# Kernel tuning notes

Hardware: AMD Instinct MI355X
Metric: run time of the kernel (lower is better)

## Reference

```python
import jax, jax.numpy as jnp
import numpy as np
import math

N = 30000        # nodes
E = 390000       # edges (first N are self-loops, in node order)
H = 64
NNS = 4          # num_node_states
NES = 4          # num_edge_states
NGRAPH = 64      # graphs in batch
TEMP_ON_EVAL = 1.0


def from_binary(bits):
    # bits: [..., k] of {0,1} -> integer code sum(bits * 2^k)
    pw = (2 ** jnp.arange(bits.shape[-1])).astype(bits.dtype)
    return jnp.sum(bits * pw, axis=-1)


def segment_softmax(logits, seg, num_seg, tau):
    m = jax.ops.segment_max(logits, seg, num_segments=num_seg)
    e = jnp.exp((logits - m[seg]) / tau)
    s = jax.ops.segment_sum(e, seg, num_segments=num_seg)
    return e / s[seg]


def segment_hard_onehot(logits, seg, num_seg):
    # gumbel_softmax with tau=0, no noise: one-hot at per-segment argmax (first on ties)
    n = logits.shape[0]
    m = jax.ops.segment_max(logits, seg, num_segments=num_seg)
    idx = jnp.where(logits >= m[seg], jnp.arange(n, dtype=jnp.int32), jnp.int32(n))
    first = jax.ops.segment_min(idx, seg, num_segments=num_seg)
    return (jnp.arange(n, dtype=jnp.int32) == first[seg]).astype(jnp.int32)


def select_best(emb, bits, scalars, index, num_index):
    # SelectBest with use_select_best=True. states are even ints < 2^(k+1);
    # unique((states, index)) groups == fused key states*num_index+index.
    states = 2 * from_binary(bits)
    key = states * num_index + index
    num_key = (2 ** (bits.shape[-1] + 1)) * num_index
    best = segment_hard_onehot(-scalars[:, 0], key, num_key)
    return emb[states + best]


def temp_by_step(step, upper, lower, num_iter, temp_on_eval):
    if step == -1:
        return temp_on_eval
    frac = min(float(step) / num_iter, 1.0)
    return upper + (lower - upper) * frac


def forward(node_states, edge_states, scalars, edge_index, batch_vec, rev_idx,
            emb_edge, emb_sbv, emb_sbr, emb_static,
            Wq, Wk, Wv, Wek, Wev, Wc, training_step):
    ei0, ei1 = edge_index[0], edge_index[1]
    # self-loop edges are the first N edges in node order ->
    # scalars[edge_index[0]==edge_index[1]] == scalars[:N]
    node_scalars = scalars[:N]                                   # [N,1]

    # select_best_from_virtual
    node_fts = select_best(emb_sbv, node_states, node_scalars, batch_vec, NGRAPH)  # [N,H]
    edge_fts = emb_edge[from_binary(edge_states)]                # [E,H]

    Q = node_fts @ Wq.T
    K = node_fts @ Wk.T
    V = node_fts @ Wv.T

    # combined_edge_KV
    sb = select_best(emb_sbr, node_states[ei0], scalars, ei1, N)  # [E,H]
    edge_K = sb @ Wek.T
    sender_s = node_scalars[ei0]                                  # [E,1]
    reciever_s = node_scalars[ei1]                                # [E,1]
    rlx = (scalars < reciever_s)
    rlx_d = (sender_s + scalars < reciever_s)
    fts = jnp.concatenate([rlx, rlx_d], axis=-1).astype(jnp.int32)  # [E,2] bits
    static_fts = emb_static[from_binary(fts)]                     # [E,H]
    combined = jnp.concatenate([edge_fts, edge_fts[rev_idx], static_fts], axis=1)  # [E,3H]
    edge_V = combined @ Wc.T                                      # [E,H]

    # compute_message
    Qe = Q[ei1]
    Ke = K[ei0] + edge_K
    Ve = V[ei0] + edge_V
    alpha = jnp.sum(Qe * Ke, axis=-1) / math.sqrt(H)              # [E]
    tau = temp_by_step(int(training_step), 3.0, 0.1, 10000, TEMP_ON_EVAL)
    alpha = segment_softmax(alpha, ei1, N, tau)
    message = Ve * alpha[:, None]                                  # [E,H]

    node_out = node_fts + jax.ops.segment_sum(message, ei1, num_segments=N)
    edge_out = edge_fts + message
    return node_out, edge_out


def setup_inputs() -> dict:
    key = jax.random.key(0)
    ks = jax.random.split(key, 16)
    node_states = jax.random.randint(ks[0], (N, NNS), 0, 2, dtype=jnp.int32)
    edge_states = jax.random.randint(ks[1], (E, NES), 0, 2, dtype=jnp.int32)
    scalars = jax.random.normal(ks[2], (E, 1), dtype=jnp.float32)
    loops = jnp.arange(N, dtype=jnp.int32)
    senders = jax.random.randint(ks[3], (E - N,), 0, N, dtype=jnp.int32)
    receivers = jax.random.randint(ks[4], (E - N,), 0, N, dtype=jnp.int32)
    edge_index = jnp.stack([jnp.concatenate([loops, senders]),
                            jnp.concatenate([loops, receivers])])  # [2,E]
    batch_vec = jnp.sort(jax.random.randint(ks[5], (N,), 0, NGRAPH, dtype=jnp.int32))
    rev_idx = jax.random.permutation(ks[6], E).astype(jnp.int32)
    s = 0.05
    return {
        'node_states': node_states, 'edge_states': edge_states, 'scalars': scalars,
        'edge_index': edge_index, 'batch_vec': batch_vec, 'rev_idx': rev_idx,
        'emb_edge': s * jax.random.normal(ks[7], (2 ** NES, H), dtype=jnp.float32),
        'emb_sbv': s * jax.random.normal(ks[8], (2 ** (NNS + 1), H), dtype=jnp.float32),
        'emb_sbr': s * jax.random.normal(ks[9], (2 ** (NNS + 1), H), dtype=jnp.float32),
        'emb_static': s * jax.random.normal(ks[10], (4, H), dtype=jnp.float32),
        'Wq': s * jax.random.normal(ks[11], (H, H), dtype=jnp.float32),
        'Wk': s * jax.random.normal(ks[12], (H, H), dtype=jnp.float32),
        'Wv': s * jax.random.normal(ks[13], (H, H), dtype=jnp.float32),
        'Wek': s * jax.random.normal(ks[14], (H, H), dtype=jnp.float32),
        'Wev': s * jax.random.normal(ks[15], (H, H), dtype=jnp.float32),
        'Wc': s * jax.random.normal(jax.random.fold_in(key, 99), (H, 3 * H), dtype=jnp.float32),
        'training_step': -1,
    }


def reference(node_states, edge_states, scalars, edge_index, batch_vec, rev_idx,
              emb_edge, emb_sbv, emb_sbr, emb_static,
              Wq, Wk, Wv, Wek, Wev, Wc, training_step):
    return forward(node_states, edge_states, scalars, edge_index, batch_vec, rev_idx,
                   emb_edge, emb_sbv, emb_sbr, emb_static,
                   Wq, Wk, Wv, Wek, Wev, Wc, training_step)
```

## Files before the change

kernel.cpp:

```cpp
#include <hip/hip_runtime.h>

#define NN 30000
#define NE 390000
#define HH 64
#define NGRAPH 64
#define AGG_BLOCKS 1024
#define NE_BLK 1524
#define NN_BLK 118

__device__ __forceinline__ unsigned sortable_f32(float f) {
    unsigned u = __float_as_uint(f);
    return (u & 0x80000000u) ? ~u : (u | 0x80000000u);
}

#define T_V   0
#define T_C1  2048
#define T_C2  3072
#define T_C3  4096
#define T_A   4352
#define T_B   5376
#define T_Q   6400
#define T_K   8448
#define T_EK  10496

__global__ __launch_bounds__(256) void k_init(
        const int4* __restrict__ edge_states, const int4* __restrict__ node_states,
        const float* __restrict__ emb_sbv, const float* __restrict__ emb_sbr,
        const float* __restrict__ emb_edge, const float* __restrict__ emb_static,
        const float* __restrict__ Wq, const float* __restrict__ Wk,
        const float* __restrict__ Wv, const float* __restrict__ Wek,
        const float* __restrict__ Wc,
        unsigned char* __restrict__ esi, int* __restrict__ ns,
        unsigned* __restrict__ cnt, unsigned long long* __restrict__ nodeSel,
        float* __restrict__ tabs) {
    int b = blockIdx.x, t = threadIdx.x;
    if (b < NE_BLK) {
        int e = b * 256 + t;
        if (e < NE) {
            int4 v = edge_states[e];
            esi[e] = (unsigned char)(v.x + 2*v.y + 4*v.z + 8*v.w);
        }
    } else if (b < NE_BLK + NN_BLK) {
        int i = (b - NE_BLK) * 256 + t;
        if (i < NN) {
            int4 v = node_states[i];
            ns[i] = 2 * (v.x + 2*v.y + 4*v.z + 8*v.w);
            cnt[i] = 0u;
        }
    } else if (b < NE_BLK + NN_BLK + 41) {
        int idx = (b - NE_BLK - NN_BLK) * 256 + t;
        if (idx >= 10496) return;
        float acc = 0.f;
        if (idx < 2048) {
            int r = idx >> 6, h = idx & 63;
            for (int j = 0; j < 64; ++j) acc += emb_sbv[r*64+j] * Wv[h*64+j];
            tabs[T_V + idx] = acc;
        } else if (idx < 3072) {
            int x = idx - 2048; int r = x >> 6, h = x & 63;
            for (int j = 0; j < 64; ++j) acc += emb_edge[r*64+j] * Wc[h*192+j];
            tabs[T_C1 + x] = acc;
        } else if (idx < 4096) {
            int x = idx - 3072; int r = x >> 6, h = x & 63;
            for (int j = 0; j < 64; ++j) acc += emb_edge[r*64+j] * Wc[h*192+64+j];
            tabs[T_C2 + x] = acc;
        } else if (idx < 4352) {
            int x = idx - 4096; int r = x >> 6, h = x & 63;
            for (int j = 0; j < 64; ++j) acc += emb_static[r*64+j] * Wc[h*192+128+j];
            tabs[T_C3 + x] = acc;
        } else if (idx < 6400) {
            int x = idx - 4352; int r = x >> 6, h = x & 63;
            for (int j = 0; j < 64; ++j) acc += emb_sbv[r*64+j] * Wq[h*64+j];
            tabs[T_Q + x] = acc;
        } else if (idx < 8448) {
            int x = idx - 6400; int r = x >> 6, h = x & 63;
            for (int j = 0; j < 64; ++j) acc += emb_sbv[r*64+j] * Wk[h*64+j];
            tabs[T_K + x] = acc;
        } else {
            int x = idx - 8448; int r = x >> 6, h = x & 63;
            for (int j = 0; j < 64; ++j) acc += emb_sbr[r*64+j] * Wek[h*64+j];
            tabs[T_EK + x] = acc;
        }
    } else {
        #pragma unroll
        for (int k = 0; k < 4; ++k) nodeSel[t * 4 + k] = ~0ull;
    }
}

__global__ __launch_bounds__(256) void k_phase2(
        const int* __restrict__ ei1, unsigned* __restrict__ cnt,
        unsigned* __restrict__ rank, const int* __restrict__ ns,
        const int* __restrict__ batch_vec, const float* __restrict__ scalars,
        unsigned long long* __restrict__ nodeSel, float* __restrict__ tabs) {
    int b = blockIdx.x, t = threadIdx.x;
    if (b < NE_BLK) {
        int e = b * 256 + t;
        if (e < NE) rank[e] = atomicAdd(&cnt[ei1[e]], 1u);
    } else if (b < NE_BLK + NN_BLK) {
        int i = (b - NE_BLK) * 256 + t;
        if (i < NN) {
            int st = ns[i];
            int key = (st >> 1) * NGRAPH + batch_vec[i];
            unsigned long long pk = ((unsigned long long)sortable_f32(scalars[i]) << 32) | (unsigned)i;
            atomicMin(&nodeSel[key], pk);
        }
    } else {
        int idx = (b - NE_BLK - NN_BLK) * 256 + t;
        if (idx >= 2048) return;
        const float* TQ = tabs + T_Q;
        float acc = 0.f;
        if (idx < 1024) {
            int r1 = idx >> 5, r0 = idx & 31;
            const float* TK = tabs + T_K;
            for (int j = 0; j < 64; ++j) acc += TQ[r1*64+j] * TK[r0*64+j];
            tabs[T_A + idx] = acc * 0.125f;
        } else {
            int x = idx - 1024; int r1 = x >> 5, rk = x & 31;
            const float* TEK = tabs + T_EK;
            for (int j = 0; j < 64; ++j) acc += TQ[r1*64+j] * TEK[rk*64+j];
            tabs[T_B + x] = acc * 0.125f;
        }
    }
}

__global__ __launch_bounds__(256) void k_phase3(
        const unsigned* __restrict__ cnt, unsigned* __restrict__ bsum,
        const int* __restrict__ ns, const int* __restrict__ batch_vec,
        const unsigned long long* __restrict__ nodeSel,
        const float* __restrict__ scalars, uint2* __restrict__ nodePk) {
    int b = blockIdx.x, t = threadIdx.x;
    if (b < NN_BLK) {
        __shared__ unsigned red[256];
        int i = b * 256 + t;
        red[t] = (i < NN) ? cnt[i] : 0u;
        __syncthreads();
        for (int o = 128; o > 0; o >>= 1) {
            if (t < o) red[t] += red[t + o];
            __syncthreads();
        }
        if (t == 0) bsum[b] = red[0];
    } else {
        int i = (b - NN_BLK) * 256 + t;
        if (i < NN) {
            int st = ns[i];
            int key = (st >> 1) * NGRAPH + batch_vec[i];
            unsigned win = (unsigned)(nodeSel[key] & 0xffffffffull);
            unsigned row = (unsigned)st + (win == (unsigned)i ? 1u : 0u);
            nodePk[i] = make_uint2(row, __float_as_uint(scalars[i]));
        }
    }
}

__global__ __launch_bounds__(128) void k_sscan(const unsigned* __restrict__ bsum,
                                               unsigned* __restrict__ bbase,
                                               unsigned* __restrict__ base) {
    __shared__ unsigned s[128];
    int t = threadIdx.x;
    unsigned v = (t < NN_BLK) ? bsum[t] : 0u;
    s[t] = v;
    __syncthreads();
    for (int o = 1; o < 128; o <<= 1) {
        unsigned u = (t >= o) ? s[t - o] : 0u;
        __syncthreads();
        s[t] += u;
        __syncthreads();
    }
    if (t < NN_BLK) bbase[t] = s[t] - v;
    if (t == 127) { bbase[NN_BLK] = s[127]; base[NN] = s[127]; }
}

__global__ __launch_bounds__(256) void k_base(const unsigned* __restrict__ cnt,
        const unsigned* __restrict__ bbase, unsigned* __restrict__ base) {
    __shared__ unsigned s[256];
    int t = threadIdx.x;
    int i = blockIdx.x * 256 + t;
    unsigned v = (i < NN) ? cnt[i] : 0u;
    s[t] = v;
    __syncthreads();
    for (int o = 1; o < 256; o <<= 1) {
        unsigned u = (t >= o) ? s[t - o] : 0u;
        __syncthreads();
        s[t] += u;
        __syncthreads();
    }
    if (i < NN) base[i] = bbase[blockIdx.x] + s[t] - v;
}

__global__ __launch_bounds__(256) void k_edge2(const int* __restrict__ ei0,
        const int* __restrict__ ei1, const uint2* __restrict__ nodePk,
        const unsigned char* __restrict__ esi, const int* __restrict__ rev_idx,
        const float* __restrict__ scalars, const unsigned* __restrict__ base,
        const unsigned* __restrict__ rank, uint2* __restrict__ sKey,
        float* __restrict__ sScal) {
    int e = blockIdx.x * 256 + threadIdx.x;
    if (e >= NE) return;
    int s0 = ei0[e], s1 = ei1[e];
    uint2 np = nodePk[s0];
    unsigned es = esi[e];
    unsigned esr = esi[rev_idx[e]];
    unsigned pos = base[s1] + rank[e];
    sKey[pos] = make_uint2((unsigned)e | (np.x << 19) | (es << 24) | (esr << 28), np.y);
    sScal[pos] = scalars[e];
}

__global__ __launch_bounds__(256) void k_agg(
        const unsigned* __restrict__ base, const uint2* __restrict__ sKey,
        const float* __restrict__ sScal, const uint2* __restrict__ nodePk,
        const float* __restrict__ tabs, const float* __restrict__ emb_edge,
        const float* __restrict__ emb_sbv, const int* __restrict__ step_ptr,
        float* __restrict__ out_node, float* __restrict__ out_edge) {
    __shared__ float lds[9472];
    __shared__ unsigned scr[4][32];
    int tid = threadIdx.x;
    for (int j = tid; j < 6400; j += 256) lds[j] = tabs[j];
    for (int j = tid; j < 1024; j += 256) lds[6400 + j] = emb_edge[j];
    for (int j = tid; j < 2048; j += 256) lds[7424 + j] = emb_sbv[j];
    __syncthreads();
    int step = step_ptr[0];
    float invTau;
    if (step == -1) invTau = 1.0f;
    else { float frac = fminf((float)step / 10000.f, 1.f); invTau = 1.0f / (3.0f + (0.1f - 3.0f) * frac); }
    int wid = tid >> 6, lane = tid & 63;
    unsigned* mySc = scr[wid];
    unsigned* myE  = scr[wid] + 16;
    int q = lane >> 4, cidx = (lane & 15) << 2;
    for (int i = blockIdx.x * 4 + wid; i < NN; i += AGG_BLOCKS * 4) {
        unsigned j0 = base[i], j1 = base[i + 1];
        int d = (int)(j1 - j0);
        uint2 np = nodePk[i];
        int r1 = (int)np.x;
        float recv = __uint_as_float(np.y);
        const float* Arow = lds + T_A + r1 * 32;
        const float* Brow = lds + T_B + r1 * 32;
        float4 acc = {0.f, 0.f, 0.f, 0.f};
        if (lane < 16) { mySc[lane] = 0xffffffffu; myE[lane] = 0xffffffffu; }
        __builtin_amdgcn_sched_barrier(0);
        if (d > 0 && d <= 64) {
            bool act = lane < d;
            uint2 key = act ? sKey[j0 + lane] : make_uint2(0u, 0u);
            float sc  = act ? sScal[j0 + lane] : 0.f;
            unsigned scs = sortable_f32(sc);
            unsigned g = (key.x >> 20) & 15u;
            unsigned e19 = key.x & 0x7ffffu;
            if (act) atomicMin(&mySc[g], scs);
            __builtin_amdgcn_sched_barrier(0);
            unsigned ms = mySc[g];
            if (act && scs == ms) atomicMin(&myE[g], e19);
            __builtin_amdgcn_sched_barrier(0);
            bool win = act && (myE[g] == e19);
            int r0 = (key.x >> 19) & 31;
            int ekrow = (r0 & 30) + (win ? 1 : 0);
            float ex = act ? __expf((Arow[r0] + Brow[ekrow]) * invTau) : 0.f;
            float send = __uint_as_float(key.y);
            int si = (sc < recv ? 1 : 0) + (send + sc < recv ? 2 : 0);
            float s = ex;
            #pragma unroll
            for (int o = 1; o < 64; o <<= 1) s += __shfl_xor(s, o);
            float p = ex / s;
            int nIt = (d + 3) >> 2;
            for (int it = 0; it < nIt; ++it) {
                int jj = it * 4 + q;
                unsigned kx = __shfl(key.x, jj);
                int sii = __shfl(si, jj);
                float pp = __shfl(p, jj);
                if (jj < d) {
                    unsigned e = kx & 0x7ffffu;
                    int rr0 = (kx >> 19) & 31, es = (kx >> 24) & 15, esr = (kx >> 28) & 15;
                    float4 tv = *(const float4*)&lds[(rr0 << 6) + cidx];
                    float4 c1 = *(const float4*)&lds[T_C1 + (es << 6) + cidx];
                    float4 c2 = *(const float4*)&lds[T_C2 + (esr << 6) + cidx];
                    float4 c3 = *(const float4*)&lds[T_C3 + (sii << 6) + cidx];
                    float4 ee = *(const float4*)&lds[6400 + (es << 6) + cidx];
                    float4 o;
                    o.x = pp * (tv.x + c1.x + c2.x + c3.x);
                    o.y = pp * (tv.y + c1.y + c2.y + c3.y);
                    o.z = pp * (tv.z + c1.z + c2.z + c3.z);
                    o.w = pp * (tv.w + c1.w + c2.w + c3.w);
                    acc.x += o.x; acc.y += o.y; acc.z += o.z; acc.w += o.w;
                    o.x += ee.x; o.y += ee.y; o.z += ee.z; o.w += ee.w;
                    *(float4*)&out_edge[(size_t)e * 64 + cidx] = o;
                }
            }
        } else if (d > 64) {
            for (unsigned c = j0; c < j1; c += 64) {
                unsigned j = c + lane;
                if (j < j1) {
                    uint2 key = sKey[j];
                    atomicMin(&mySc[(key.x >> 20) & 15u], sortable_f32(sScal[j]));
                }
            }
            __builtin_amdgcn_sched_barrier(0);
            for (unsigned c = j0; c < j1; c += 64) {
                unsigned j = c + lane;
                if (j < j1) {
                    uint2 key = sKey[j];
                    unsigned g = (key.x >> 20) & 15u;
                    if (sortable_f32(sScal[j]) == mySc[g]) atomicMin(&myE[g], key.x & 0x7ffffu);
                }
            }
            __builtin_amdgcn_sched_barrier(0);
            float s = 0.f;
            for (unsigned c = j0; c < j1; c += 64) {
                unsigned j = c + lane;
                if (j < j1) {
                    uint2 key = sKey[j];
                    bool win = (myE[(key.x >> 20) & 15u] == (key.x & 0x7ffffu));
                    int r0 = (key.x >> 19) & 31;
                    int ekrow = (r0 & 30) + (win ? 1 : 0);
                    s += __expf((Arow[r0] + Brow[ekrow]) * invTau);
                }
            }
            #pragma unroll
            for (int o = 1; o < 64; o <<= 1) s += __shfl_xor(s, o);
            float invS = 1.f / s;
            for (unsigned c = j0; c < j1; c += 4) {
                unsigned j = c + q;
                if (j < j1) {
                    uint2 key = sKey[j];
                    float sc = sScal[j];
                    bool win = (myE[(key.x >> 20) & 15u] == (key.x & 0x7ffffu));
                    int r0 = (key.x >> 19) & 31;
                    int ekrow = (r0 & 30) + (win ? 1 : 0);
                    float pp = __expf((Arow[r0] + Brow[ekrow]) * invTau) * invS;
                    float send = __uint_as_float(key.y);
                    int si = (sc < recv ? 1 : 0) + (send + sc < recv ? 2 : 0);
                    unsigned e = key.x & 0x7ffffu;
                    int es = (key.x >> 24) & 15, esr = (key.x >> 28) & 15;
                    float4 tv = *(const float4*)&lds[(r0 << 6) + cidx];
                    float4 c1 = *(const float4*)&lds[T_C1 + (es << 6) + cidx];
                    float4 c2 = *(const float4*)&lds[T_C2 + (esr << 6) + cidx];
                    float4 c3 = *(const float4*)&lds[T_C3 + (si << 6) + cidx];
                    float4 ee = *(const float4*)&lds[6400 + (es << 6) + cidx];
                    float4 o;
                    o.x = pp * (tv.x + c1.x + c2.x + c3.x);
                    o.y = pp * (tv.y + c1.y + c2.y + c3.y);
                    o.z = pp * (tv.z + c1.z + c2.z + c3.z);
                    o.w = pp * (tv.w + c1.w + c2.w + c3.w);
                    acc.x += o.x; acc.y += o.y; acc.z += o.z; acc.w += o.w;
                    o.x += ee.x; o.y += ee.y; o.z += ee.z; o.w += ee.w;
                    *(float4*)&out_edge[(size_t)e * 64 + cidx] = o;
                }
            }
        }
        acc.x += __shfl_xor(acc.x, 16); acc.y += __shfl_xor(acc.y, 16);
        acc.z += __shfl_xor(acc.z, 16); acc.w += __shfl_xor(acc.w, 16);
        acc.x += __shfl_xor(acc.x, 32); acc.y += __shfl_xor(acc.y, 32);
        acc.z += __shfl_xor(acc.z, 32); acc.w += __shfl_xor(acc.w, 32);
        if (lane < 16) {
            float4 nb = *(const float4*)&lds[7424 + (r1 << 6) + cidx];
            float4 o;
            o.x = nb.x + acc.x; o.y = nb.y + acc.y; o.z = nb.z + acc.z; o.w = nb.w + acc.w;
            *(float4*)&out_node[(size_t)i * 64 + cidx] = o;
        }
    }
}

extern "C" void kernel_launch(void* const* d_in, const int* in_sizes, int n_in,
                              void* d_out, int out_size, void* d_ws, size_t ws_size,
                              hipStream_t stream) {
    const int4*  node_states = (const int4*)d_in[0];
    const int4*  edge_states = (const int4*)d_in[1];
    const float* scalars     = (const float*)d_in[2];
    const int*   edge_index  = (const int*)d_in[3];
    const int*   batch_vec   = (const int*)d_in[4];
    const int*   rev_idx     = (const int*)d_in[5];
    const float* emb_edge    = (const float*)d_in[6];
    const float* emb_sbv     = (const float*)d_in[7];
    const float* emb_sbr     = (const float*)d_in[8];
    const float* emb_static  = (const float*)d_in[9];
    const float* Wq  = (const float*)d_in[10];
    const float* Wk  = (const float*)d_in[11];
    const float* Wv  = (const float*)d_in[12];
    const float* Wek = (const float*)d_in[13];
    const float* Wc  = (const float*)d_in[15];
    const int*   step = (const int*)d_in[16];

    const int* ei0 = edge_index;
    const int* ei1 = edge_index + NE;

    char* ws = (char*)d_ws;
    int*      ns     = (int*)(ws);
    uint2*    nodePk = (uint2*)(ws + 120000);
    unsigned char* esi = (unsigned char*)(ws + 360000);
    unsigned* rank   = (unsigned*)(ws + 750016);
    unsigned* cnt    = (unsigned*)(ws + 2310016);
    unsigned* baseA  = (unsigned*)(ws + 2430080);
    uint2*    sKey   = (uint2*)(ws + 2550144);
    float*    sScal  = (float*)(ws + 5670144);
    unsigned long long* nodeSel = (unsigned long long*)(ws + 7230144);
    float*    tabs   = (float*)(ws + 7238336);
    unsigned* bsum   = (unsigned*)(ws + 7288512);
    unsigned* bbase  = (unsigned*)(ws + 7289024);

    float* out_node = (float*)d_out;
    float* out_edge = out_node + (size_t)NN * HH;

    hipLaunchKernelGGL(k_init, dim3(NE_BLK + NN_BLK + 41 + 1), dim3(256), 0, stream,
                       edge_states, node_states, emb_sbv, emb_sbr, emb_edge, emb_static,
                       Wq, Wk, Wv, Wek, Wc, esi, ns, cnt, nodeSel, tabs);
    hipLaunchKernelGGL(k_phase2, dim3(NE_BLK + NN_BLK + 8), dim3(256), 0, stream,
                       ei1, cnt, rank, ns, batch_vec, scalars, nodeSel, tabs);
    hipLaunchKernelGGL(k_phase3, dim3(NN_BLK * 2), dim3(256), 0, stream,
                       cnt, bsum, ns, batch_vec, nodeSel, scalars, nodePk);
    hipLaunchKernelGGL(k_sscan, dim3(1), dim3(128), 0, stream, bsum, bbase, baseA);
    hipLaunchKernelGGL(k_base, dim3(NN_BLK), dim3(256), 0, stream, cnt, bbase, baseA);
    hipLaunchKernelGGL(k_edge2, dim3(NE_BLK), dim3(256), 0, stream,
                       ei0, ei1, nodePk, esi, rev_idx, scalars, baseA, rank, sKey, sScal);
    hipLaunchKernelGGL(k_agg, dim3(AGG_BLOCKS), dim3(256), 0, stream,
                       baseA, sKey, sScal, nodePk, tabs, emb_edge, emb_sbv, step,
                       out_node, out_edge);
}
```

Measured before the change: 77.44 us.

## Move edge output writes to a coalesced pass and fuse the CSR scan

The aggregation kernel no longer writes the 100MB edge output scattered in receiver-sorted order. It stores a packed per-edge probability and state word, and a new final kernel writes out_edge coalesced in edge order. The three scan kernels are merged into one, where each block recomputes its prefix by summing all earlier counts. This adds an extra kernel, extra per-edge metadata traffic, and redundant prefix reads in exchange for coalesced output writes and fewer launches. Packing si into the low 2 bits of p slightly perturbs the probability value.

```diff
diff --git a/kernel.cpp b/kernel.cpp
--- a/kernel.cpp
+++ b/kernel.cpp
@@ -5,6 +5,7 @@
 #define HH 64
 #define NGRAPH 64
 #define AGG_BLOCKS 1024
+#define FIN_BLOCKS 2048
 #define NE_BLK 1524
 #define NN_BLK 118
 
@@ -122,22 +123,37 @@
     }
 }
 
-__global__ __launch_bounds__(256) void k_phase3(
-        const unsigned* __restrict__ cnt, unsigned* __restrict__ bsum,
+__global__ __launch_bounds__(256) void k_csr(
+        const unsigned* __restrict__ cnt, unsigned* __restrict__ base,
         const int* __restrict__ ns, const int* __restrict__ batch_vec,
         const unsigned long long* __restrict__ nodeSel,
         const float* __restrict__ scalars, uint2* __restrict__ nodePk) {
     int b = blockIdx.x, t = threadIdx.x;
     if (b < NN_BLK) {
         __shared__ unsigned red[256];
-        int i = b * 256 + t;
-        red[t] = (i < NN) ? cnt[i] : 0u;
+        __shared__ unsigned sc[256];
+        unsigned pre = 0;
+        int lim = b * 256;
+        for (int j = t; j < lim; j += 256) pre += cnt[j];
+        red[t] = pre;
         __syncthreads();
         for (int o = 128; o > 0; o >>= 1) {
             if (t < o) red[t] += red[t + o];
             __syncthreads();
         }
-        if (t == 0) bsum[b] = red[0];
+        unsigned P = red[0];
+        int i = lim + t;
+        unsigned v = (i < NN) ? cnt[i] : 0u;
+        sc[t] = v;
+        __syncthreads();
+        for (int o = 1; o < 256; o <<= 1) {
+            unsigned u = (t >= o) ? sc[t - o] : 0u;
+            __syncthreads();
+            sc[t] += u;
+            __syncthreads();
+        }
+        if (i < NN) base[i] = P + sc[t] - v;
+        if (b == NN_BLK - 1 && t == 255) base[NN] = P + sc[255];
     } else {
         int i = (b - NN_BLK) * 256 + t;
         if (i < NN) {
@@ -150,47 +166,12 @@
     }
 }
 
-__global__ __launch_bounds__(128) void k_sscan(const unsigned* __restrict__ bsum,
-                                               unsigned* __restrict__ bbase,
-                                               unsigned* __restrict__ base) {
-    __shared__ unsigned s[128];
-    int t = threadIdx.x;
-    unsigned v = (t < NN_BLK) ? bsum[t] : 0u;
-    s[t] = v;
-    __syncthreads();
-    for (int o = 1; o < 128; o <<= 1) {
-        unsigned u = (t >= o) ? s[t - o] : 0u;
-        __syncthreads();
-        s[t] += u;
-        __syncthreads();
-    }
-    if (t < NN_BLK) bbase[t] = s[t] - v;
-    if (t == 127) { bbase[NN_BLK] = s[127]; base[NN] = s[127]; }
-}
-
-__global__ __launch_bounds__(256) void k_base(const unsigned* __restrict__ cnt,
-        const unsigned* __restrict__ bbase, unsigned* __restrict__ base) {
-    __shared__ unsigned s[256];
-    int t = threadIdx.x;
-    int i = blockIdx.x * 256 + t;
-    unsigned v = (i < NN) ? cnt[i] : 0u;
-    s[t] = v;
-    __syncthreads();
-    for (int o = 1; o < 256; o <<= 1) {
-        unsigned u = (t >= o) ? s[t - o] : 0u;
-        __syncthreads();
-        s[t] += u;
-        __syncthreads();
-    }
-    if (i < NN) base[i] = bbase[blockIdx.x] + s[t] - v;
-}
-
 __global__ __launch_bounds__(256) void k_edge2(const int* __restrict__ ei0,
         const int* __restrict__ ei1, const uint2* __restrict__ nodePk,
         const unsigned char* __restrict__ esi, const int* __restrict__ rev_idx,
         const float* __restrict__ scalars, const unsigned* __restrict__ base,
         const unsigned* __restrict__ rank, uint2* __restrict__ sKey,
-        float* __restrict__ sScal) {
+        float* __restrict__ sScal, unsigned* __restrict__ einfoE) {
     int e = blockIdx.x * 256 + threadIdx.x;
     if (e >= NE) return;
     int s0 = ei0[e], s1 = ei1[e];
@@ -200,20 +181,20 @@
     unsigned pos = base[s1] + rank[e];
     sKey[pos] = make_uint2((unsigned)e | (np.x << 19) | (es << 24) | (esr << 28), np.y);
     sScal[pos] = scalars[e];
+    einfoE[e] = np.x | (es << 5) | (esr << 9);
 }
 
 __global__ __launch_bounds__(256) void k_agg(
         const unsigned* __restrict__ base, const uint2* __restrict__ sKey,
         const float* __restrict__ sScal, const uint2* __restrict__ nodePk,
-        const float* __restrict__ tabs, const float* __restrict__ emb_edge,
-        const float* __restrict__ emb_sbv, const int* __restrict__ step_ptr,
-        float* __restrict__ out_node, float* __restrict__ out_edge) {
-    __shared__ float lds[9472];
+        const float* __restrict__ tabs, const float* __restrict__ emb_sbv,
+        const int* __restrict__ step_ptr, unsigned* __restrict__ pe,
+        float* __restrict__ out_node) {
+    __shared__ float lds[8448];
     __shared__ unsigned scr[4][32];
     int tid = threadIdx.x;
     for (int j = tid; j < 6400; j += 256) lds[j] = tabs[j];
-    for (int j = tid; j < 1024; j += 256) lds[6400 + j] = emb_edge[j];
-    for (int j = tid; j < 2048; j += 256) lds[7424 + j] = emb_sbv[j];
+    for (int j = tid; j < 2048; j += 256) lds[6400 + j] = emb_sbv[j];
     __syncthreads();
     int step = step_ptr[0];
     float invTau;
@@ -256,6 +237,7 @@
             #pragma unroll
             for (int o = 1; o < 64; o <<= 1) s += __shfl_xor(s, o);
             float p = ex / s;
+            if (act) pe[e19] = (__float_as_uint(p) & ~3u) | (unsigned)si;
             int nIt = (d + 3) >> 2;
             for (int it = 0; it < nIt; ++it) {
                 int jj = it * 4 + q;
@@ -263,21 +245,15 @@
                 int sii = __shfl(si, jj);
                 float pp = __shfl(p, jj);
                 if (jj < d) {
-                    unsigned e = kx & 0x7ffffu;
                     int rr0 = (kx >> 19) & 31, es = (kx >> 24) & 15, esr = (kx >> 28) & 15;
                     float4 tv = *(const float4*)&lds[(rr0 << 6) + cidx];
                     float4 c1 = *(const float4*)&lds[T_C1 + (es << 6) + cidx];
                     float4 c2 = *(const float4*)&lds[T_C2 + (esr << 6) + cidx];
                     float4 c3 = *(const float4*)&lds[T_C3 + (sii << 6) + cidx];
-                    float4 ee = *(const float4*)&lds[6400 + (es << 6) + cidx];
-                    float4 o;
-                    o.x = pp * (tv.x + c1.x + c2.x + c3.x);
-                    o.y = pp * (tv.y + c1.y + c2.y + c3.y);
-                    o.z = pp * (tv.z + c1.z + c2.z + c3.z);
-                    o.w = pp * (tv.w + c1.w + c2.w + c3.w);
-                    acc.x += o.x; acc.y += o.y; acc.z += o.z; acc.w += o.w;
-                    o.x += ee.x; o.y += ee.y; o.z += ee.z; o.w += ee.w;
-                    *(float4*)&out_edge[(size_t)e * 64 + cidx] = o;
+                    acc.x += pp * (tv.x + c1.x + c2.x + c3.x);
+                    acc.y += pp * (tv.y + c1.y + c2.y + c3.y);
+                    acc.z += pp * (tv.z + c1.z + c2.z + c3.z);
+                    acc.w += pp * (tv.w + c1.w + c2.w + c3.w);
                 }
             }
         } else if (d > 64) {
@@ -325,19 +301,15 @@
                     int si = (sc < recv ? 1 : 0) + (send + sc < recv ? 2 : 0);
                     unsigned e = key.x & 0x7ffffu;
                     int es = (key.x >> 24) & 15, esr = (key.x >> 28) & 15;
+                    if ((lane & 15) == 0) pe[e] = (__float_as_uint(pp) & ~3u) | (unsigned)si;
                     float4 tv = *(const float4*)&lds[(r0 << 6) + cidx];
                     float4 c1 = *(const float4*)&lds[T_C1 + (es << 6) + cidx];
                     float4 c2 = *(const float4*)&lds[T_C2 + (esr << 6) + cidx];
                     float4 c3 = *(const float4*)&lds[T_C3 + (si << 6) + cidx];
-                    float4 ee = *(const float4*)&lds[6400 + (es << 6) + cidx];
-                    float4 o;
-                    o.x = pp * (tv.x + c1.x + c2.x + c3.x);
-                    o.y = pp * (tv.y + c1.y + c2.y + c3.y);
-                    o.z = pp * (tv.z + c1.z + c2.z + c3.z);
-                    o.w = pp * (tv.w + c1.w + c2.w + c3.w);
-                    acc.x += o.x; acc.y += o.y; acc.z += o.z; acc.w += o.w;
-                    o.x += ee.x; o.y += ee.y; o.z += ee.z; o.w += ee.w;
-                    *(float4*)&out_edge[(size_t)e * 64 + cidx] = o;
+                    acc.x += pp * (tv.x + c1.x + c2.x + c3.x);
+                    acc.y += pp * (tv.y + c1.y + c2.y + c3.y);
+                    acc.z += pp * (tv.z + c1.z + c2.z + c3.z);
+                    acc.w += pp * (tv.w + c1.w + c2.w + c3.w);
                 }
             }
         }
@@ -346,11 +318,46 @@
         acc.x += __shfl_xor(acc.x, 32); acc.y += __shfl_xor(acc.y, 32);
         acc.z += __shfl_xor(acc.z, 32); acc.w += __shfl_xor(acc.w, 32);
         if (lane < 16) {
-            float4 nb = *(const float4*)&lds[7424 + (r1 << 6) + cidx];
+            float4 nb = *(const float4*)&lds[6400 + (r1 << 6) + cidx];
             float4 o;
             o.x = nb.x + acc.x; o.y = nb.y + acc.y; o.z = nb.z + acc.z; o.w = nb.w + acc.w;
             *(float4*)&out_node[(size_t)i * 64 + cidx] = o;
         }
+    }
+}
+
+__global__ __launch_bounds__(256) void k_final(
+        const unsigned* __restrict__ einfoE, const unsigned* __restrict__ pe,
+        const float* __restrict__ tabs, const float* __restrict__ emb_edge,
+        float* __restrict__ out_edge) {
+    __shared__ float lds[5376];
+    int tid = threadIdx.x;
+    for (int j = tid; j < 4352; j += 256) lds[j] = tabs[j];
+    for (int j = tid; j < 1024; j += 256) lds[4352 + j] = emb_edge[j];
+    __syncthreads();
+    int lane = tid & 63;
+    int q = lane >> 4, c4 = (lane & 15) << 2;
+    int gw = (blockIdx.x * 256 + tid) >> 6;
+    const int NQ = NE / 4;
+    const int NW = FIN_BLOCKS * 4;
+    for (int quad = gw; quad < NQ; quad += NW) {
+        int e = (quad << 2) + q;
+        unsigned info = einfoE[e];
+        unsigned u = pe[e];
+        float p = __uint_as_float(u & ~3u);
+        int si = (int)(u & 3u);
+        int r0 = info & 31, es = (info >> 5) & 15, esr = (info >> 9) & 15;
+        float4 tv = *(const float4*)&lds[(r0 << 6) + c4];
+        float4 c1 = *(const float4*)&lds[T_C1 + (es << 6) + c4];
+        float4 c2 = *(const float4*)&lds[T_C2 + (esr << 6) + c4];
+        float4 c3 = *(const float4*)&lds[T_C3 + (si << 6) + c4];
+        float4 ee = *(const float4*)&lds[4352 + (es << 6) + c4];
+        float4 o;
+        o.x = ee.x + p * (tv.x + c1.x + c2.x + c3.x);
+        o.y = ee.y + p * (tv.y + c1.y + c2.y + c3.y);
+        o.z = ee.z + p * (tv.z + c1.z + c2.z + c3.z);
+        o.w = ee.w + p * (tv.w + c1.w + c2.w + c3.w);
+        *(float4*)&out_edge[(size_t)e * 64 + c4] = o;
     }
 }
 
@@ -388,8 +395,8 @@
     float*    sScal  = (float*)(ws + 5670144);
     unsigned long long* nodeSel = (unsigned long long*)(ws + 7230144);
     float*    tabs   = (float*)(ws + 7238336);
-    unsigned* bsum   = (unsigned*)(ws + 7288512);
-    unsigned* bbase  = (unsigned*)(ws + 7289024);
+    unsigned* einfoE = (unsigned*)(ws + 7288512);
+    unsigned* pe     = (unsigned*)(ws + 8848512);
 
     float* out_node = (float*)d_out;
     float* out_edge = out_node + (size_t)NN * HH;
@@ -399,13 +406,13 @@
                        Wq, Wk, Wv, Wek, Wc, esi, ns, cnt, nodeSel, tabs);
     hipLaunchKernelGGL(k_phase2, dim3(NE_BLK + NN_BLK + 8), dim3(256), 0, stream,
                        ei1, cnt, rank, ns, batch_vec, scalars, nodeSel, tabs);
-    hipLaunchKernelGGL(k_phase3, dim3(NN_BLK * 2), dim3(256), 0, stream,
-                       cnt, bsum, ns, batch_vec, nodeSel, scalars, nodePk);
-    hipLaunchKernelGGL(k_sscan, dim3(1), dim3(128), 0, stream, bsum, bbase, baseA);
-    hipLaunchKernelGGL(k_base, dim3(NN_BLK), dim3(256), 0, stream, cnt, bbase, baseA);
+    hipLaunchKernelGGL(k_csr, dim3(NN_BLK * 2), dim3(256), 0, stream,
+                       cnt, baseA, ns, batch_vec, nodeSel, scalars, nodePk);
     hipLaunchKernelGGL(k_edge2, dim3(NE_BLK), dim3(256), 0, stream,
-                       ei0, ei1, nodePk, esi, rev_idx, scalars, baseA, rank, sKey, sScal);
+                       ei0, ei1, nodePk, esi, rev_idx, scalars, baseA, rank,
+                       sKey, sScal, einfoE);
     hipLaunchKernelGGL(k_agg, dim3(AGG_BLOCKS), dim3(256), 0, stream,
-                       baseA, sKey, sScal, nodePk, tabs, emb_edge, emb_sbv, step,
-                       out_node, out_edge);
-}
+                       baseA, sKey, sScal, nodePk, tabs, emb_sbv, step, pe, out_node);
+    hipLaunchKernelGGL(k_final, dim3(FIN_BLOCKS), dim3(256), 0, stream,
+                       einfoE, pe, tabs, emb_edge, out_edge);
+}
```

Measured after the change: 110.8 us. 1.43x slower.

## Fuse three-kernel prefix scan into one redundant-prefix kernel, shrink agg LDS

Applied to the files above, without the earlier changes.

Each scan block now recomputes its own global prefix by summing all preceding counts and then does a local scan. This replaces the block-sum, single-block scan and base kernels with one kernel and removes two launches and their dependencies. The aggregation kernel no longer stages emb_sbv in LDS and reads it from global memory instead. That lowers LDS use, which may allow more resident blocks, and the grid grows from 1024 to 1280 blocks. In exchange, later scan blocks do quadratic redundant reads of cnt.

```diff
diff --git a/kernel.cpp b/kernel.cpp
--- a/kernel.cpp
+++ b/kernel.cpp
@@ -4,7 +4,7 @@
 #define NE 390000
 #define HH 64
 #define NGRAPH 64
-#define AGG_BLOCKS 1024
+#define AGG_BLOCKS 1280
 #define NE_BLK 1524
 #define NN_BLK 118
 
@@ -122,22 +122,37 @@
     }
 }
 
-__global__ __launch_bounds__(256) void k_phase3(
-        const unsigned* __restrict__ cnt, unsigned* __restrict__ bsum,
+__global__ __launch_bounds__(256) void k_csr(
+        const unsigned* __restrict__ cnt, unsigned* __restrict__ base,
         const int* __restrict__ ns, const int* __restrict__ batch_vec,
         const unsigned long long* __restrict__ nodeSel,
         const float* __restrict__ scalars, uint2* __restrict__ nodePk) {
     int b = blockIdx.x, t = threadIdx.x;
     if (b < NN_BLK) {
         __shared__ unsigned red[256];
-        int i = b * 256 + t;
-        red[t] = (i < NN) ? cnt[i] : 0u;
+        __shared__ unsigned sc[256];
+        unsigned pre = 0;
+        int lim = b * 256;
+        for (int j = t; j < lim; j += 256) pre += cnt[j];
+        red[t] = pre;
         __syncthreads();
         for (int o = 128; o > 0; o >>= 1) {
             if (t < o) red[t] += red[t + o];
             __syncthreads();
         }
-        if (t == 0) bsum[b] = red[0];
+        unsigned P = red[0];
+        int i = lim + t;
+        unsigned v = (i < NN) ? cnt[i] : 0u;
+        sc[t] = v;
+        __syncthreads();
+        for (int o = 1; o < 256; o <<= 1) {
+            unsigned u = (t >= o) ? sc[t - o] : 0u;
+            __syncthreads();
+            sc[t] += u;
+            __syncthreads();
+        }
+        if (i < NN) base[i] = P + sc[t] - v;
+        if (b == NN_BLK - 1 && t == 255) base[NN] = P + sc[255];
     } else {
         int i = (b - NN_BLK) * 256 + t;
         if (i < NN) {
@@ -148,41 +163,6 @@
             nodePk[i] = make_uint2(row, __float_as_uint(scalars[i]));
         }
     }
-}
-
-__global__ __launch_bounds__(128) void k_sscan(const unsigned* __restrict__ bsum,
-                                               unsigned* __restrict__ bbase,
-                                               unsigned* __restrict__ base) {
-    __shared__ unsigned s[128];
-    int t = threadIdx.x;
-    unsigned v = (t < NN_BLK) ? bsum[t] : 0u;
-    s[t] = v;
-    __syncthreads();
-    for (int o = 1; o < 128; o <<= 1) {
-        unsigned u = (t >= o) ? s[t - o] : 0u;
-        __syncthreads();
-        s[t] += u;
-        __syncthreads();
-    }
-    if (t < NN_BLK) bbase[t] = s[t] - v;
-    if (t == 127) { bbase[NN_BLK] = s[127]; base[NN] = s[127]; }
-}
-
-__global__ __launch_bounds__(256) void k_base(const unsigned* __restrict__ cnt,
-        const unsigned* __restrict__ bbase, unsigned* __restrict__ base) {
-    __shared__ unsigned s[256];
-    int t = threadIdx.x;
-    int i = blockIdx.x * 256 + t;
-    unsigned v = (i < NN) ? cnt[i] : 0u;
-    s[t] = v;
-    __syncthreads();
-    for (int o = 1; o < 256; o <<= 1) {
-        unsigned u = (t >= o) ? s[t - o] : 0u;
-        __syncthreads();
-        s[t] += u;
-        __syncthreads();
-    }
-    if (i < NN) base[i] = bbase[blockIdx.x] + s[t] - v;
 }
 
 __global__ __launch_bounds__(256) void k_edge2(const int* __restrict__ ei0,
@@ -208,12 +188,11 @@
         const float* __restrict__ tabs, const float* __restrict__ emb_edge,
         const float* __restrict__ emb_sbv, const int* __restrict__ step_ptr,
         float* __restrict__ out_node, float* __restrict__ out_edge) {
-    __shared__ float lds[9472];
+    __shared__ float lds[7424];
     __shared__ unsigned scr[4][32];
     int tid = threadIdx.x;
     for (int j = tid; j < 6400; j += 256) lds[j] = tabs[j];
     for (int j = tid; j < 1024; j += 256) lds[6400 + j] = emb_edge[j];
-    for (int j = tid; j < 2048; j += 256) lds[7424 + j] = emb_sbv[j];
     __syncthreads();
     int step = step_ptr[0];
     float invTau;
@@ -346,7 +325,7 @@
         acc.x += __shfl_xor(acc.x, 32); acc.y += __shfl_xor(acc.y, 32);
         acc.z += __shfl_xor(acc.z, 32); acc.w += __shfl_xor(acc.w, 32);
         if (lane < 16) {
-            float4 nb = *(const float4*)&lds[7424 + (r1 << 6) + cidx];
+            float4 nb = *(const float4*)&emb_sbv[(r1 << 6) + cidx];
             float4 o;
             o.x = nb.x + acc.x; o.y = nb.y + acc.y; o.z = nb.z + acc.z; o.w = nb.w + acc.w;
             *(float4*)&out_node[(size_t)i * 64 + cidx] = o;
@@ -388,8 +367,6 @@
     float*    sScal  = (float*)(ws + 5670144);
     unsigned long long* nodeSel = (unsigned long long*)(ws + 7230144);
     float*    tabs   = (float*)(ws + 7238336);
-    unsigned* bsum   = (unsigned*)(ws + 7288512);
-    unsigned* bbase  = (unsigned*)(ws + 7289024);
 
     float* out_node = (float*)d_out;
     float* out_edge = out_node + (size_t)NN * HH;
@@ -399,10 +376,8 @@
                        Wq, Wk, Wv, Wek, Wc, esi, ns, cnt, nodeSel, tabs);
     hipLaunchKernelGGL(k_phase2, dim3(NE_BLK + NN_BLK + 8), dim3(256), 0, stream,
                        ei1, cnt, rank, ns, batch_vec, scalars, nodeSel, tabs);
-    hipLaunchKernelGGL(k_phase3, dim3(NN_BLK * 2), dim3(256), 0, stream,
-                       cnt, bsum, ns, batch_vec, nodeSel, scalars, nodePk);
-    hipLaunchKernelGGL(k_sscan, dim3(1), dim3(128), 0, stream, bsum, bbase, baseA);
-    hipLaunchKernelGGL(k_base, dim3(NN_BLK), dim3(256), 0, stream, cnt, bbase, baseA);
+    hipLaunchKernelGGL(k_csr, dim3(NN_BLK * 2), dim3(256), 0, stream,
+                       cnt, baseA, ns, batch_vec, nodeSel, scalars, nodePk);
     hipLaunchKernelGGL(k_edge2, dim3(NE_BLK), dim3(256), 0, stream,
                        ei0, ei1, nodePk, esi, rev_idx, scalars, baseA, rank, sKey, sScal);
     hipLaunchKernelGGL(k_agg, dim3(AGG_BLOCKS), dim3(256), 0, stream,
```

Result: slower. 87.72 us (+13.3%).
